# Performance work log

Hardware: AMD Instinct MI355X
Metric: run time of the kernel (lower is better)

## Reference

```python
import jax, jax.numpy as jnp
import numpy as np

B, S, H, T = 32, 512, 1024, 32


def setup_inputs() -> dict:
    key = jax.random.key(0)
    ks = jax.random.split(key, 8)
    hidden = jax.random.normal(ks[0], (B, S, H), dtype=jnp.float32)
    W = jax.random.normal(ks[1], (H, T), dtype=jnp.float32) * 0.02
    b = jax.random.normal(ks[2], (T,), dtype=jnp.float32) * 0.02
    start_trans = jax.random.normal(ks[3], (T,), dtype=jnp.float32) * 0.1
    end_trans = jax.random.normal(ks[4], (T,), dtype=jnp.float32) * 0.1
    trans = jax.random.normal(ks[5], (T, T), dtype=jnp.float32) * 0.1
    tags = jax.random.randint(ks[6], (B, S), 0, T, dtype=jnp.int64)
    # variable-length mask: first position always valid (CRF requirement)
    lengths = jax.random.randint(ks[7], (B,), S // 2, S + 1)
    mask = jnp.arange(S)[None, :] < lengths[:, None]  # [B,S] bool
    return {"hidden": hidden, "W": W, "b": b, "start_trans": start_trans,
            "end_trans": end_trans, "trans": trans, "tags": tags, "mask": mask}


def reference(hidden, W, b, start_trans, end_trans, trans, tags, mask):
    # emission = log_softmax(fc(last_hidden_state))  [B,S,T]
    emissions = jax.nn.log_softmax(jnp.einsum('bsh,ht->bst', hidden, W) + b, axis=-1)
    maskf = mask.astype(emissions.dtype)

    # --- numerator: score of the gold tag path ---
    emit_tag = jnp.take_along_axis(emissions, tags[..., None], axis=-1)[..., 0]  # [B,S]
    trans_tag = trans[tags[:, :-1], tags[:, 1:]]                                  # [B,S-1]
    num = (start_trans[tags[:, 0]]
           + (emit_tag * maskf).sum(axis=1)
           + (trans_tag * maskf[:, 1:]).sum(axis=1))
    seq_len = mask.sum(axis=1).astype(jnp.int32)                                  # [B]
    last_tags = jnp.take_along_axis(tags, (seq_len - 1)[:, None].astype(tags.dtype), axis=1)[:, 0]
    num = num + end_trans[last_tags]

    # --- denominator: forward algorithm (masked logsumexp recurrence) ---
    alpha0 = start_trans[None, :] + emissions[:, 0]  # [B,T]

    def step(alpha, inp):
        em_t, m_t = inp  # [B,T], [B]
        nxt = jax.nn.logsumexp(alpha[:, :, None] + trans[None] + em_t[:, None, :], axis=1)
        return jnp.where(m_t[:, None], nxt, alpha), None

    em_rest = jnp.moveaxis(emissions[:, 1:], 1, 0)  # [S-1,B,T]
    m_rest = jnp.moveaxis(mask[:, 1:], 1, 0)        # [S-1,B]
    alpha, _ = jax.lax.scan(step, alpha0, (em_rest, m_rest))
    denom = jax.nn.logsumexp(alpha + end_trans[None], axis=1)  # [B]

    llh = num - denom        # CRF returns per-batch log-likelihood
    return -llh.mean()       # loss = (-crf(...)).mean()
```

## Files before the change

kernel.cpp:

```cpp
#include <hip/hip_runtime.h>
#include <hip/hip_bf16.h>


#define Bb 32
#define Ss 512
#define Hh 1024
#define Tt 32
#define NROWS (Bb*Ss)
#define NCHUNK 32
#define CHUNK_L 16

typedef __attribute__((ext_vector_type(8))) short bf16x8;
typedef __attribute__((ext_vector_type(4))) float f32x4;

__device__ __forceinline__ short f2bf(float f) {
  union { float f; unsigned u; } v; v.f = f;
  unsigned u = v.u;
  return (short)((u + 0x7FFFu + ((u >> 16) & 1u)) >> 16);
}

__global__ __launch_bounds__(1024) void wpack_kernel(
    const float* __restrict__ W, short* __restrict__ Wpk,
    float* __restrict__ out) {
  const int k = threadIdx.x;
  if (k == 0) out[0] = 0.f;
#pragma unroll
  for (int t = 0; t < 32; ++t)
    Wpk[t * Hh + k] = f2bf(W[k * 32 + t]);
}

__global__ __launch_bounds__(256) void emis_fused_kernel(
    const float* __restrict__ hidden, const short* __restrict__ Wpk,
    const float* __restrict__ bias, float* __restrict__ logem,
    float* __restrict__ pem) {
  __shared__ __align__(16) char smem[32768];
  float* red = (float*)smem;
  const int tid = threadIdx.x;
  const int wv = tid >> 6, lane = tid & 63;
  const int n = lane & 15, q = lane >> 4;
  const int row0 = blockIdx.x * 16;
  const int koff = wv * 256;

  {
    const int swv = tid >> 6;
    const int skc = (tid >> 3) & 7;
    const int sq = (tid >> 1) & 3;
    const int sj0 = (tid & 1) * 4;
    const int rbase = swv * 8192 + skc * 1024 + sj0 * 2;
    const int uxor = skc * 32;
    const float* hp = hidden + (size_t)row0 * Hh + 4 * tid;
#pragma unroll
    for (int i = 0; i < 16; ++i) {
      const float4 v = *(const float4*)(hp + (size_t)i * Hh);
      uint2 u;
      u.x = (unsigned short)f2bf(v.x) | ((unsigned)(unsigned short)f2bf(v.y) << 16);
      u.y = (unsigned short)f2bf(v.z) | ((unsigned)(unsigned short)f2bf(v.w) << 16);
      const int unit = ((i * 4 + sq) * 16) ^ uxor;
      *(uint2*)(smem + rbase + unit - sj0 * 2 + sj0 * 2 + (unit ? 0 : 0)) = u;
    }
  }
  __syncthreads();

  const short* bpl = Wpk + n * Hh + koff;
  const short* bpr = Wpk + (16 + n) * Hh + koff;
  f32x4 d0 = {0.f, 0.f, 0.f, 0.f}, d1 = {0.f, 0.f, 0.f, 0.f};
#pragma unroll
  for (int kc = 0; kc < 8; ++kc) {
    const int aaddr = wv * 8192 + kc * 1024 + (((n * 4 + q) * 16) ^ (kc * 32));
    const bf16x8 a = *(const bf16x8*)(smem + aaddr);
    const bf16x8 wl = *(const bf16x8*)(bpl + kc * 32 + 8 * q);
    const bf16x8 wr = *(const bf16x8*)(bpr + kc * 32 + 8 * q);
    d0 = __builtin_amdgcn_mfma_f32_16x16x32_bf16(a, wl, d0, 0, 0, 0);
    d1 = __builtin_amdgcn_mfma_f32_16x16x32_bf16(a, wr, d1, 0, 0, 0);
  }
  __syncthreads();

#pragma unroll
  for (int r = 0; r < 4; ++r) {
    red[(wv * 16 + 4 * q + r) * 33 + n] = d0[r];
    red[(wv * 16 + 4 * q + r) * 33 + 16 + n] = d1[r];
  }
  __syncthreads();

  const int row = tid >> 4, c0 = tid & 15, c1 = 16 + c0;
  float v0 = 0.f, v1 = 0.f;
#pragma unroll
  for (int w = 0; w < 4; ++w) {
    v0 += red[(w * 16 + row) * 33 + c0];
    v1 += red[(w * 16 + row) * 33 + c1];
  }
  const float L0 = v0 + bias[c0], L1 = v1 + bias[c1];
  float mx = fmaxf(L0, L1);
#pragma unroll
  for (int d = 8; d >= 1; d >>= 1) mx = fmaxf(mx, __shfl_xor(mx, d, 16));
  float se = __expf(L0 - mx) + __expf(L1 - mx);
#pragma unroll
  for (int d = 8; d >= 1; d >>= 1) se += __shfl_xor(se, d, 16);
  const float corr = mx + __logf(se);
  const float lg0 = L0 - corr, lg1 = L1 - corr;
  const size_t rb = (size_t)(row0 + row) * Tt;
  logem[rb + c0] = lg0;
  logem[rb + c1] = lg1;
  pem[rb + c0] = __expf(lg0);
  pem[rb + c1] = __expf(lg1);
}

__global__ __launch_bounds__(256) void chunk_kernel(
    const float* __restrict__ pem, const float* __restrict__ trans,
    const int* __restrict__ mask, float* __restrict__ ecT,
    float* __restrict__ moff) {
  __shared__ __align__(16) float Pbuf[4 * 32 * 36];
  const int tid = threadIdx.x;
  const int wv = tid >> 6, lane = tid & 63;
  const int n = lane & 15, q = lane >> 4;
  const int chunk = blockIdx.x * 4 + wv;
  const int b = chunk >> 5, cc = chunk & 31;
  float* P = Pbuf + wv * 32 * 36;

  float etr0[8], etr1[8];
#pragma unroll
  for (int jj = 0; jj < 8; ++jj) {
    etr0[jj] = __expf(trans[(8 * q + jj) * 32 + n]);
    etr1[jj] = __expf(trans[(8 * q + jj) * 32 + 16 + n]);
  }

  const int t0 = 1 + cc * CHUNK_L;
  const int rowbase = b * Ss + t0;
  int pred = 0;
  if (lane < 16 && t0 + lane < Ss) pred = mask[rowbase + lane];
  const unsigned long long bal = __ballot(pred != 0);
  const int nst = __popcll(bal & 0xFFFFull);

  bf16x8 a0, a1;
#pragma unroll
  for (int jj = 0; jj < 8; ++jj) {
    a0[jj] = (n == 8 * q + jj) ? (short)0x3F80 : (short)0;
    a1[jj] = (16 + n == 8 * q + jj) ? (short)0x3F80 : (short)0;
  }

  f32x4 d00, d01, d10, d11;
  if (nst == 0) {
#pragma unroll
    for (int r = 0; r < 4; ++r) {
      d00[r] = (4 * q + r == n) ? 1.f : 0.f;
      d01[r] = 0.f;
      d10[r] = 0.f;
      d11[r] = (4 * q + r == n) ? 1.f : 0.f;
    }
  }
  float em0 = 0.f, em1 = 0.f;
  if (nst > 0) {
    em0 = pem[(size_t)rowbase * Tt + n];
    em1 = pem[(size_t)rowbase * Tt + 16 + n];
  }
  for (int st = 0; st < nst; ++st) {
    float em0n = 0.f, em1n = 0.f;
    if (st + 1 < nst) {
      em0n = pem[(size_t)(rowbase + st + 1) * Tt + n];
      em1n = pem[(size_t)(rowbase + st + 1) * Tt + 16 + n];
    }
    bf16x8 bL, bR;
#pragma unroll
    for (int jj = 0; jj < 8; ++jj) {
      bL[jj] = f2bf(etr0[jj] * em0);
      bR[jj] = f2bf(etr1[jj] * em1);
    }
    const f32x4 z = {0.f, 0.f, 0.f, 0.f};
    d00 = __builtin_amdgcn_mfma_f32_16x16x32_bf16(a0, bL, z, 0, 0, 0);
    d01 = __builtin_amdgcn_mfma_f32_16x16x32_bf16(a0, bR, z, 0, 0, 0);
    d10 = __builtin_amdgcn_mfma_f32_16x16x32_bf16(a1, bL, z, 0, 0, 0);
    d11 = __builtin_amdgcn_mfma_f32_16x16x32_bf16(a1, bR, z, 0, 0, 0);
    if (st + 1 < nst) {
#pragma unroll
      for (int r = 0; r < 4; ++r) {
        P[(4 * q + r) * 36 + n] = d00[r];
        P[(4 * q + r) * 36 + 16 + n] = d01[r];
        P[(16 + 4 * q + r) * 36 + n] = d10[r];
        P[(16 + 4 * q + r) * 36 + 16 + n] = d11[r];
      }
      __builtin_amdgcn_s_waitcnt(0);
      const float4 lo0 = *(const float4*)&P[n * 36 + 8 * q];
      const float4 lo1 = *(const float4*)&P[n * 36 + 8 * q + 4];
      const float4 hi0 = *(const float4*)&P[(16 + n) * 36 + 8 * q];
      const float4 hi1 = *(const float4*)&P[(16 + n) * 36 + 8 * q + 4];
      a0[0] = f2bf(lo0.x); a0[1] = f2bf(lo0.y); a0[2] = f2bf(lo0.z); a0[3] = f2bf(lo0.w);
      a0[4] = f2bf(lo1.x); a0[5] = f2bf(lo1.y); a0[6] = f2bf(lo1.z); a0[7] = f2bf(lo1.w);
      a1[0] = f2bf(hi0.x); a1[1] = f2bf(hi0.y); a1[2] = f2bf(hi0.z); a1[3] = f2bf(hi0.w);
      a1[4] = f2bf(hi1.x); a1[5] = f2bf(hi1.y); a1[6] = f2bf(hi1.z); a1[7] = f2bf(hi1.w);
    }
    em0 = em0n; em1 = em1n;
  }

  float lg0[4], lg1[4], iv0[4], iv1[4];
#pragma unroll
  for (int r = 0; r < 4; ++r) {
    float m0v = fmaxf(d00[r], d01[r]);
    float m1v = fmaxf(d10[r], d11[r]);
#pragma unroll
    for (int d = 8; d >= 1; d >>= 1) {
      m0v = fmaxf(m0v, __shfl_xor(m0v, d, 16));
      m1v = fmaxf(m1v, __shfl_xor(m1v, d, 16));
    }
    m0v = fmaxf(m0v, 1e-37f);
    m1v = fmaxf(m1v, 1e-37f);
    lg0[r] = __logf(m0v); iv0[r] = __builtin_amdgcn_rcpf(m0v);
    lg1[r] = __logf(m1v); iv1[r] = __builtin_amdgcn_rcpf(m1v);
  }
  float* E = ecT + (size_t)(b * NCHUNK + cc) * 32 * 32;
  {
    float4 s;
    s = make_float4(d00[0] * iv0[0], d00[1] * iv0[1], d00[2] * iv0[2], d00[3] * iv0[3]);
    *(float4*)&E[n * 32 + 4 * q] = s;
    s = make_float4(d10[0] * iv1[0], d10[1] * iv1[1], d10[2] * iv1[2], d10[3] * iv1[3]);
    *(float4*)&E[n * 32 + 16 + 4 * q] = s;
    s = make_float4(d01[0] * iv0[0], d01[1] * iv0[1], d01[2] * iv0[2], d01[3] * iv0[3]);
    *(float4*)&E[(16 + n) * 32 + 4 * q] = s;
    s = make_float4(d11[0] * iv1[0], d11[1] * iv1[1], d11[2] * iv1[2], d11[3] * iv1[3]);
    *(float4*)&E[(16 + n) * 32 + 16 + 4 * q] = s;
  }
  if (n == 0) {
    float* Mo = moff + (size_t)(b * NCHUNK + cc) * 32;
    *(float4*)&Mo[4 * q] = make_float4(lg0[0], lg0[1], lg0[2], lg0[3]);
    *(float4*)&Mo[16 + 4 * q] = make_float4(lg1[0], lg1[1], lg1[2], lg1[3]);
  }
}

__global__ __launch_bounds__(64) void phase2_kernel(
    const float* __restrict__ logem, const float* __restrict__ start_trans,
    const float* __restrict__ end_trans, const float* __restrict__ ecT,
    const float* __restrict__ moff, const float* __restrict__ trans,
    const int* __restrict__ tags, const int* __restrict__ mask,
    float* __restrict__ out) {
  const int b = blockIdx.x;
  const int lane = threadIdx.x;
  const int j = lane & 31;
  __shared__ __align__(16) float qlds[32];

  const int base_row = b * Ss;
  int lensum = 0;
  float snum = 0.f;
#pragma unroll
  for (int k = 0; k < 8; ++k) {
    const int ss = lane + 64 * k;
    const int m = mask[base_row + ss];
    lensum += m;
    if (m) {
      const int tg = tags[base_row + ss];
      snum += logem[(size_t)(base_row + ss) * Tt + tg];
      if (ss > 0) snum += trans[tags[base_row + ss - 1] * Tt + tg];
    }
  }
#pragma unroll
  for (int d = 32; d >= 1; d >>= 1) {
    snum += __shfl_xor(snum, d);
    lensum += __shfl_xor(lensum, d);
  }

  const float* base = ecT + (size_t)b * NCHUNK * 32 * 32;
  const float* mbase = moff + (size_t)b * NCHUNK * 32;

  float4 M[8], N[8];
  const float* r0 = base + j * 32;
#pragma unroll
  for (int k = 0; k < 8; ++k) M[k] = *(const float4*)(r0 + 4 * k);
  float mo_cur = mbase[j];

  float al0 = start_trans[j] + logem[(size_t)base_row * Tt + j];
  float m0 = al0;
#pragma unroll
  for (int d = 16; d >= 1; d >>= 1) m0 = fmaxf(m0, __shfl_xor(m0, d, 32));
  float a = __expf(al0 - m0);
  float Mb = m0;
  const float eend = __expf(end_trans[j]);

  float mo_next = 0.f;
  for (int c = 0; c < NCHUNK; ++c) {
    if (c + 1 < NCHUNK) {
      const float* rn = base + ((c + 1) * 32 + j) * 32;
#pragma unroll
      for (int k = 0; k < 8; ++k) N[k] = *(const float4*)(rn + 4 * k);
      mo_next = mbase[(c + 1) * 32 + j];
    }
    float mom = mo_cur;
#pragma unroll
    for (int d = 16; d >= 1; d >>= 1) mom = fmaxf(mom, __shfl_xor(mom, d, 32));
    float qv = a * __expf(mo_cur - mom);
    if (lane < 32) qlds[j] = qv;
    __builtin_amdgcn_s_waitcnt(0);
    float s = 0.f;
#pragma unroll
    for (int k = 0; k < 8; ++k) {
      const float4 q4 = *(const float4*)(qlds + 4 * k);
      s = fmaf(q4.x, M[k].x, s);
      s = fmaf(q4.y, M[k].y, s);
      s = fmaf(q4.z, M[k].z, s);
      s = fmaf(q4.w, M[k].w, s);
    }
    float m = s;
#pragma unroll
    for (int d = 16; d >= 1; d >>= 1) m = fmaxf(m, __shfl_xor(m, d, 32));
    m = fmaxf(m, 1e-30f);
    a = s * __builtin_amdgcn_rcpf(m);
    Mb += mom + __logf(m);
#pragma unroll
    for (int k = 0; k < 8; ++k) M[k] = N[k];
    mo_cur = mo_next;
  }
  float z = a * eend;
#pragma unroll
  for (int d = 16; d >= 1; d >>= 1) z += __shfl_xor(z, d, 32);
  if (lane == 0) {
    const float numfull = snum + start_trans[tags[base_row]] +
                          end_trans[tags[base_row + lensum - 1]];
    const float denom = Mb + __logf(z);
    atomicAdd(out, -(numfull - denom) * (1.0f / 32.0f));
  }
}

extern "C" void kernel_launch(void* const* d_in, const int* in_sizes, int n_in,
                              void* d_out, int out_size, void* d_ws, size_t ws_size,
                              hipStream_t stream) {
  const float* hidden = (const float*)d_in[0];
  const float* W = (const float*)d_in[1];
  const float* bias = (const float*)d_in[2];
  const float* start_trans = (const float*)d_in[3];
  const float* end_trans = (const float*)d_in[4];
  const float* trans = (const float*)d_in[5];
  const int* tags = (const int*)d_in[6];
  const int* mask = (const int*)d_in[7];
  float* out = (float*)d_out;

  float* logem = (float*)d_ws;
  float* pem = logem + (size_t)NROWS * Tt;
  float* ecT = pem + (size_t)NROWS * Tt;
  float* moff = ecT + (size_t)Bb * NCHUNK * 32 * 32;
  short* Wpk = (short*)(moff + (size_t)Bb * NCHUNK * 32);

  wpack_kernel<<<1, 1024, 0, stream>>>(W, Wpk, out);
  emis_fused_kernel<<<NROWS / 16, 256, 0, stream>>>(hidden, Wpk, bias, logem, pem);
  chunk_kernel<<<Bb * NCHUNK / 4, 256, 0, stream>>>(pem, trans, mask, ecT, moff);
  phase2_kernel<<<Bb, 64, 0, stream>>>(logem, start_trans, end_trans, ecT, moff,
                                       trans, tags, mask, out);
}
```

Baseline: 165.4 us.

## Drop pem buffer, precompute chunk maxima, and lazily renormalize phase2 recurrence

Removes the separate exp(emission) buffer so the emission kernel writes only log-emissions, and the chunk kernel computes exp on the fly. The chunk kernel also writes a per-chunk max of its offsets, so phase2 reads it with a shuffle instead of running a max-reduction every step. Phase2 splits the dot product into four accumulators and renormalizes only every fourth chunk. The weight-pack kernel is spread over 8 blocks, and the LDS waits are narrowed to lgkmcnt. Skipping renormalization for several chunks risks overflow or underflow in fp32.

```diff
diff --git a/kernel.cpp b/kernel.cpp
--- a/kernel.cpp
+++ b/kernel.cpp
@@ -19,10 +19,10 @@
   return (short)((u + 0x7FFFu + ((u >> 16) & 1u)) >> 16);
 }
 
-__global__ __launch_bounds__(1024) void wpack_kernel(
+__global__ __launch_bounds__(128) void wpack_kernel(
     const float* __restrict__ W, short* __restrict__ Wpk,
     float* __restrict__ out) {
-  const int k = threadIdx.x;
+  const int k = blockIdx.x * 128 + threadIdx.x;
   if (k == 0) out[0] = 0.f;
 #pragma unroll
   for (int t = 0; t < 32; ++t)
@@ -31,8 +31,7 @@
 
 __global__ __launch_bounds__(256) void emis_fused_kernel(
     const float* __restrict__ hidden, const short* __restrict__ Wpk,
-    const float* __restrict__ bias, float* __restrict__ logem,
-    float* __restrict__ pem) {
+    const float* __restrict__ bias, float* __restrict__ logem) {
   __shared__ __align__(16) char smem[32768];
   float* red = (float*)smem;
   const int tid = threadIdx.x;
@@ -56,7 +55,7 @@
       u.x = (unsigned short)f2bf(v.x) | ((unsigned)(unsigned short)f2bf(v.y) << 16);
       u.y = (unsigned short)f2bf(v.z) | ((unsigned)(unsigned short)f2bf(v.w) << 16);
       const int unit = ((i * 4 + sq) * 16) ^ uxor;
-      *(uint2*)(smem + rbase + unit - sj0 * 2 + sj0 * 2 + (unit ? 0 : 0)) = u;
+      *(uint2*)(smem + rbase + unit) = u;
     }
   }
   __syncthreads();
@@ -97,18 +96,15 @@
 #pragma unroll
   for (int d = 8; d >= 1; d >>= 1) se += __shfl_xor(se, d, 16);
   const float corr = mx + __logf(se);
-  const float lg0 = L0 - corr, lg1 = L1 - corr;
   const size_t rb = (size_t)(row0 + row) * Tt;
-  logem[rb + c0] = lg0;
-  logem[rb + c1] = lg1;
-  pem[rb + c0] = __expf(lg0);
-  pem[rb + c1] = __expf(lg1);
+  logem[rb + c0] = L0 - corr;
+  logem[rb + c1] = L1 - corr;
 }
 
 __global__ __launch_bounds__(256) void chunk_kernel(
-    const float* __restrict__ pem, const float* __restrict__ trans,
+    const float* __restrict__ logem, const float* __restrict__ trans,
     const int* __restrict__ mask, float* __restrict__ ecT,
-    float* __restrict__ moff) {
+    float* __restrict__ moff, float* __restrict__ cmax) {
   __shared__ __align__(16) float Pbuf[4 * 32 * 36];
   const int tid = threadIdx.x;
   const int wv = tid >> 6, lane = tid & 63;
@@ -150,14 +146,14 @@
   }
   float em0 = 0.f, em1 = 0.f;
   if (nst > 0) {
-    em0 = pem[(size_t)rowbase * Tt + n];
-    em1 = pem[(size_t)rowbase * Tt + 16 + n];
+    em0 = __expf(logem[(size_t)rowbase * Tt + n]);
+    em1 = __expf(logem[(size_t)rowbase * Tt + 16 + n]);
   }
   for (int st = 0; st < nst; ++st) {
     float em0n = 0.f, em1n = 0.f;
     if (st + 1 < nst) {
-      em0n = pem[(size_t)(rowbase + st + 1) * Tt + n];
-      em1n = pem[(size_t)(rowbase + st + 1) * Tt + 16 + n];
+      em0n = __expf(logem[(size_t)(rowbase + st + 1) * Tt + n]);
+      em1n = __expf(logem[(size_t)(rowbase + st + 1) * Tt + 16 + n]);
     }
     bf16x8 bL, bR;
 #pragma unroll
@@ -178,7 +174,8 @@
         P[(16 + 4 * q + r) * 36 + n] = d10[r];
         P[(16 + 4 * q + r) * 36 + 16 + n] = d11[r];
       }
-      __builtin_amdgcn_s_waitcnt(0);
+      asm volatile("s_waitcnt lgkmcnt(0)" ::: "memory");
+      __builtin_amdgcn_sched_barrier(0);
       const float4 lo0 = *(const float4*)&P[n * 36 + 8 * q];
       const float4 lo1 = *(const float4*)&P[n * 36 + 8 * q + 4];
       const float4 hi0 = *(const float4*)&P[(16 + n) * 36 + 8 * q];
@@ -223,14 +220,21 @@
     *(float4*)&Mo[4 * q] = make_float4(lg0[0], lg0[1], lg0[2], lg0[3]);
     *(float4*)&Mo[16 + 4 * q] = make_float4(lg1[0], lg1[1], lg1[2], lg1[3]);
   }
+  {
+    float cm = fmaxf(fmaxf(fmaxf(lg0[0], lg0[1]), fmaxf(lg0[2], lg0[3])),
+                     fmaxf(fmaxf(lg1[0], lg1[1]), fmaxf(lg1[2], lg1[3])));
+    cm = fmaxf(cm, __shfl_xor(cm, 16));
+    cm = fmaxf(cm, __shfl_xor(cm, 32));
+    if (lane == 0) cmax[b * NCHUNK + cc] = cm;
+  }
 }
 
 __global__ __launch_bounds__(64) void phase2_kernel(
     const float* __restrict__ logem, const float* __restrict__ start_trans,
     const float* __restrict__ end_trans, const float* __restrict__ ecT,
-    const float* __restrict__ moff, const float* __restrict__ trans,
-    const int* __restrict__ tags, const int* __restrict__ mask,
-    float* __restrict__ out) {
+    const float* __restrict__ moff, const float* __restrict__ cmax,
+    const float* __restrict__ trans, const int* __restrict__ tags,
+    const int* __restrict__ mask, float* __restrict__ out) {
   const int b = blockIdx.x;
   const int lane = threadIdx.x;
   const int j = lane & 31;
@@ -258,6 +262,7 @@
 
   const float* base = ecT + (size_t)b * NCHUNK * 32 * 32;
   const float* mbase = moff + (size_t)b * NCHUNK * 32;
+  const float cm_l = cmax[b * NCHUNK + j];
 
   float4 M[8], N[8];
   const float* r0 = base + j * 32;
@@ -281,27 +286,33 @@
       for (int k = 0; k < 8; ++k) N[k] = *(const float4*)(rn + 4 * k);
       mo_next = mbase[(c + 1) * 32 + j];
     }
-    float mom = mo_cur;
-#pragma unroll
-    for (int d = 16; d >= 1; d >>= 1) mom = fmaxf(mom, __shfl_xor(mom, d, 32));
-    float qv = a * __expf(mo_cur - mom);
+    const float mom = __shfl(cm_l, c, 32);
+    const float qv = a * __expf(mo_cur - mom);
     if (lane < 32) qlds[j] = qv;
-    __builtin_amdgcn_s_waitcnt(0);
-    float s = 0.f;
+    asm volatile("s_waitcnt lgkmcnt(0)" ::: "memory");
+    __builtin_amdgcn_sched_barrier(0);
+    float s0 = 0.f, s1 = 0.f, s2 = 0.f, s3 = 0.f;
 #pragma unroll
     for (int k = 0; k < 8; ++k) {
       const float4 q4 = *(const float4*)(qlds + 4 * k);
-      s = fmaf(q4.x, M[k].x, s);
-      s = fmaf(q4.y, M[k].y, s);
-      s = fmaf(q4.z, M[k].z, s);
-      s = fmaf(q4.w, M[k].w, s);
-    }
-    float m = s;
-#pragma unroll
-    for (int d = 16; d >= 1; d >>= 1) m = fmaxf(m, __shfl_xor(m, d, 32));
-    m = fmaxf(m, 1e-30f);
-    a = s * __builtin_amdgcn_rcpf(m);
-    Mb += mom + __logf(m);
+      float* sp = (k & 1) ? ((k & 2) ? &s3 : &s1) : ((k & 2) ? &s2 : &s0);
+      *sp = fmaf(q4.x, M[k].x, *sp);
+      *sp = fmaf(q4.y, M[k].y, *sp);
+      *sp = fmaf(q4.z, M[k].z, *sp);
+      *sp = fmaf(q4.w, M[k].w, *sp);
+    }
+    const float s = (s0 + s1) + (s2 + s3);
+    Mb += mom;
+    if ((c & 3) == 3) {
+      float m = s;
+#pragma unroll
+      for (int d = 16; d >= 1; d >>= 1) m = fmaxf(m, __shfl_xor(m, d, 32));
+      m = fmaxf(m, 1e-30f);
+      a = s * __builtin_amdgcn_rcpf(m);
+      Mb += __logf(m);
+    } else {
+      a = s;
+    }
 #pragma unroll
     for (int k = 0; k < 8; ++k) M[k] = N[k];
     mo_cur = mo_next;
@@ -331,14 +342,14 @@
   float* out = (float*)d_out;
 
   float* logem = (float*)d_ws;
-  float* pem = logem + (size_t)NROWS * Tt;
-  float* ecT = pem + (size_t)NROWS * Tt;
+  float* ecT = logem + (size_t)NROWS * Tt;
   float* moff = ecT + (size_t)Bb * NCHUNK * 32 * 32;
-  short* Wpk = (short*)(moff + (size_t)Bb * NCHUNK * 32);
-
-  wpack_kernel<<<1, 1024, 0, stream>>>(W, Wpk, out);
-  emis_fused_kernel<<<NROWS / 16, 256, 0, stream>>>(hidden, Wpk, bias, logem, pem);
-  chunk_kernel<<<Bb * NCHUNK / 4, 256, 0, stream>>>(pem, trans, mask, ecT, moff);
+  float* cmax = moff + (size_t)Bb * NCHUNK * 32;
+  short* Wpk = (short*)(cmax + (size_t)Bb * NCHUNK);
+
+  wpack_kernel<<<8, 128, 0, stream>>>(W, Wpk, out);
+  emis_fused_kernel<<<NROWS / 16, 256, 0, stream>>>(hidden, Wpk, bias, logem);
+  chunk_kernel<<<Bb * NCHUNK / 4, 256, 0, stream>>>(logem, trans, mask, ecT, moff, cmax);
   phase2_kernel<<<Bb, 64, 0, stream>>>(logem, start_trans, end_trans, ecT, moff,
-                                       trans, tags, mask, out);
-}
+                                       cmax, trans, tags, mask, out);
+}
```

Result: faster. 151.1 us (-8.7%).
